# Optimization experiments

Hardware: AMD Instinct MI355X
Metric: run time of the kernel (lower is better)

The kernel has to match this reference:

```python
import jax, jax.numpy as jnp
import numpy as np

N_HEAD = 16
QMIN, QMAX = 0.0, 255.0  # 8-bit asymmetric


def fake_quantize(x, scale, zp):
    # LearnableFakeQuantize (asymmetric, 8-bit) with straight-through round.
    q = x / scale + zp
    q = q + jax.lax.stop_gradient(jnp.round(q) - q)  # STE round
    q = jnp.clip(q, QMIN, QMAX)
    return (q - zp) * scale


def setup_inputs() -> dict:
    key = jax.random.key(0)
    ks = jax.random.split(key, 4)
    B, T, C = 2, 2048, 1024
    return {
        "hidden_states": jax.random.normal(ks[0], (B, T, C), jnp.float32),
        "W_attn": jax.random.normal(ks[1], (C, 3 * C), jnp.float32) * (1.0 / np.sqrt(C)),
        "b_attn": jnp.zeros((3 * C,), jnp.float32),
        "W_proj": jax.random.normal(ks[2], (C, C), jnp.float32) * (1.0 / np.sqrt(C)),
        "b_proj": jnp.zeros((C,), jnp.float32),
        "kv_scale": jnp.full((1,), 0.05, jnp.float32),
        "kv_zp": jnp.full((1,), 128.0, jnp.float32),
    }


def reference(hidden_states, W_attn, b_attn, W_proj, b_proj, kv_scale, kv_zp):
    B, T, C = hidden_states.shape
    H = N_HEAD
    D = C // H
    qkv = hidden_states @ W_attn + b_attn            # [B,T,3C]
    q, k, v = jnp.split(qkv, 3, axis=2)
    # [B,T,C] -> [B,H,T,D]
    q = q.reshape(B, T, H, D).transpose(0, 2, 1, 3)
    k = k.reshape(B, T, H, D).transpose(0, 2, 1, 3)
    v = v.reshape(B, T, H, D).transpose(0, 2, 1, 3)
    k = fake_quantize(k, kv_scale, kv_zp)
    v = fake_quantize(v, kv_scale, kv_zp)
    scores = jnp.einsum("bhqd,bhkd->bhqk", q, k) / jnp.sqrt(jnp.asarray(D, q.dtype))
    causal = jnp.tril(jnp.ones((T, T), bool))        # bias[:T,:T]
    scores = jnp.where(causal, scores, jnp.asarray(-jnp.inf, scores.dtype))
    attn = jax.nn.softmax(scores, axis=-1)
    out = jnp.einsum("bhqk,bhkd->bhqd", attn, v)     # [B,H,T,D]
    out = out.transpose(0, 2, 1, 3).reshape(B, T, C)
    return out @ W_proj + b_proj
```

## Files before the change

kernel.cpp:

```cpp
#include <hip/hip_runtime.h>
#include <math.h>

#define TB 2048
#define CC 1024
#define NH 16
#define HD 64

typedef __bf16 bf16x8 __attribute__((ext_vector_type(8)));
typedef __bf16 bf16x4 __attribute__((ext_vector_type(4)));
typedef float  f32x4  __attribute__((ext_vector_type(4)));

__device__ inline float exp2fast(float x) { return __builtin_amdgcn_exp2f(x); }

__device__ __forceinline__ void gl_lds16(const __bf16* g, __bf16* l) {
    __builtin_amdgcn_global_load_lds(
        (const __attribute__((address_space(1))) void*)g,
        (__attribute__((address_space(3))) void*)l, 16, 0, 0);
}

__global__ __launch_bounds__(256)
void prep_kernel(const float* __restrict__ hidden, __bf16* __restrict__ hb,
                 const float* __restrict__ Wa, __bf16* __restrict__ wat,
                 const float* __restrict__ Wp, __bf16* __restrict__ wpt)
{
    __shared__ __bf16 L[64][68];
    const int tid = threadIdx.x;
    const int bid = blockIdx.x;
    if (bid < 4096) {
        int i = (bid * 256 + tid) * 4;
        f32x4 v = *(const f32x4*)&hidden[i];
        bf16x4 o;
        o.x = (__bf16)v.x; o.y = (__bf16)v.y; o.z = (__bf16)v.z; o.w = (__bf16)v.w;
        *(bf16x4*)&hb[i] = o;
        return;
    }
    const float* src; __bf16* dst; int N, n0, k0;
    if (bid < 4096 + 768) {
        int t = bid - 4096;
        src = Wa; dst = wat; N = 3072;
        n0 = (t % 48) * 64; k0 = (t / 48) * 64;
    } else {
        int t = bid - 4864;
        src = Wp; dst = wpt; N = 1024;
        n0 = (t % 16) * 64; k0 = (t / 16) * 64;
    }
    #pragma unroll
    for (int i = 0; i < 4; i++) {
        int id = tid + i * 256;
        int r = id >> 4, c = (id & 15) * 4;
        f32x4 v = *(const f32x4*)&src[(size_t)(k0 + r) * N + n0 + c];
        bf16x4 o;
        o.x = (__bf16)v.x; o.y = (__bf16)v.y; o.z = (__bf16)v.z; o.w = (__bf16)v.w;
        *(bf16x4*)&L[r][c] = o;
    }
    __syncthreads();
    #pragma unroll
    for (int i = 0; i < 4; i++) {
        int id = tid + i * 256;
        int nr = id >> 4, kc = (id & 15) * 4;
        bf16x4 o;
        o.x = L[kc + 0][nr]; o.y = L[kc + 1][nr];
        o.z = L[kc + 2][nr]; o.w = L[kc + 3][nr];
        *(bf16x4*)&dst[(size_t)(n0 + nr) * 1024 + k0 + kc] = o;
    }
}

template<int BN, int MODE>
__global__ __launch_bounds__(256)
void gemm_bt(const __bf16* __restrict__ A, const __bf16* __restrict__ Bt,
             const float* __restrict__ bias,
             __bf16* __restrict__ o0, __bf16* __restrict__ o1,
             __bf16* __restrict__ o2, float* __restrict__ of,
             int M, int N, int K,
             const float* __restrict__ scp, const float* __restrict__ zpp)
{
    constexpr int NT = BN / 32;
    __shared__ __bf16 Asm[128][64];
    __shared__ __bf16 Bsm[BN][64];

    const int tid  = threadIdx.x;
    const int m0   = blockIdx.y * 128;
    const int n0   = blockIdx.x * BN;
    const int w    = tid >> 6, lane = tid & 63;
    const int wm   = (w & 1) * 64, wn = (w >> 1) * (BN / 2);
    const int r16  = lane & 15, quad = lane >> 4;
    const int srow = lane >> 3;
    const int scol = ((lane & 7) ^ srow) * 8;
    const int rsw  = r16 & 7;

    f32x4 acc[NT][4];
    #pragma unroll
    for (int i = 0; i < NT; i++)
        #pragma unroll
        for (int j = 0; j < 4; j++) acc[i][j] = 0.f;

    for (int k0 = 0; k0 < K; k0 += 64) {
        #pragma unroll
        for (int p = 0; p < 4; p++)
            gl_lds16(&A[(size_t)(m0 + w * 32 + p * 8 + srow) * K + k0 + scol],
                     &Asm[w * 32 + p * 8][0]);
        #pragma unroll
        for (int p = 0; p < BN / 32; p++)
            gl_lds16(&Bt[(size_t)(n0 + w * (BN / 4) + p * 8 + srow) * K + k0 + scol],
                     &Bsm[w * (BN / 4) + p * 8][0]);
        __syncthreads();

        #pragma unroll
        for (int ks = 0; ks < 2; ks++) {
            const int col = ((ks * 4 + quad) ^ rsw) * 8;
            bf16x8 af[4], bfr[NT];
            #pragma unroll
            for (int mt = 0; mt < 4; mt++)
                af[mt] = *(const bf16x8*)&Asm[wm + mt * 16 + r16][col];
            #pragma unroll
            for (int nt = 0; nt < NT; nt++)
                bfr[nt] = *(const bf16x8*)&Bsm[wn + nt * 16 + r16][col];
            #pragma unroll
            for (int nt = 0; nt < NT; nt++)
                #pragma unroll
                for (int mt = 0; mt < 4; mt++)
                    acc[nt][mt] = __builtin_amdgcn_mfma_f32_16x16x32_bf16(
                        bfr[nt], af[mt], acc[nt][mt], 0, 0, 0);
        }
        __syncthreads();
    }

    const float sc = scp[0];
    const float zp = zpp[0];

    #pragma unroll
    for (int nt = 0; nt < NT; nt++) {
        #pragma unroll
        for (int mt = 0; mt < 4; mt++) {
            int gm = m0 + wm + mt * 16 + r16;
            int gn = n0 + wn + nt * 16 + quad * 4;
            f32x4 val = acc[nt][mt] + *(const f32x4*)&bias[gn];
            if (MODE == 1) {
                *(f32x4*)&of[(size_t)gm * N + gn] = val;
            } else {
                int part = gn >> 10;
                int idx  = gn & 1023;
                int h = idx >> 6, d = idx & 63;
                int b = gm >> 11, t = gm & 2047;
                bf16x4 st;
                if (part == 0) {
                    size_t off = (((size_t)(b * NH + h)) * TB + t) * HD + d;
                    #pragma unroll
                    for (int r = 0; r < 4; r++)
                        st[r] = (__bf16)(val[r] * 0.18033688f);
                    *(bf16x4*)&o0[off] = st;
                } else {
                    #pragma unroll
                    for (int r = 0; r < 4; r++) {
                        float qv = val[r] / sc + zp;
                        qv = rintf(qv);
                        qv = fminf(fmaxf(qv, 0.f), 255.f);
                        st[r] = (__bf16)((qv - zp) * sc);
                    }
                    if (part == 1) {
                        size_t off = (((size_t)(b * NH + h)) * TB + t) * HD + d;
                        *(bf16x4*)&o1[off] = st;
                    } else {
                        size_t offv = (((size_t)(b * NH + h)) * HD + d) * TB + t;
                        #pragma unroll
                        for (int r = 0; r < 4; r++)
                            o2[offv + (size_t)r * TB] = st[r];
                    }
                }
            }
        }
    }
}

__global__ __launch_bounds__(256)
void attn_mfma(const __bf16* __restrict__ Q, const __bf16* __restrict__ Kg,
               const __bf16* __restrict__ Vt, __bf16* __restrict__ O)
{
    __shared__ alignas(16) __bf16 Ksm[64][72];
    __shared__ alignas(16) __bf16 Vsm[64][72];

    const int tid = threadIdx.x;
    const int qt  = 31 - (blockIdx.x >> 5);
    const int bh  = blockIdx.x & 31;
    const int q0  = qt * 64;
    const int w   = tid >> 6, lane = tid & 63;
    const int l15 = lane & 15, quad = lane >> 4;
    const int b   = bh >> 4, h = bh & 15;

    const int srow = tid >> 3;
    const int sseg = (tid & 7) * 8;
    const int p0 = ((srow >> 2) & 1) * 32 + ((srow >> 3) & 3) * 4 + (srow & 3);
    const int p1 = p0 + 16;

    const __bf16* Kbh = Kg + (size_t)bh * TB * HD;
    const __bf16* Vbh = Vt + (size_t)bh * HD * TB;

    const __bf16* Qrow = Q + ((size_t)bh * TB + q0 + w * 16 + l15) * HD;
    bf16x8 qf0 = *(const bf16x8*)&Qrow[quad * 8];
    bf16x8 qf1 = *(const bf16x8*)&Qrow[32 + quad * 8];

    bf16x8 af_l;
    {
        __bf16 v = (l15 == 0) ? (__bf16)1.0f : (__bf16)0.0f;
        #pragma unroll
        for (int j = 0; j < 8; j++) af_l[j] = v;
    }

    f32x4 acc_o[4], acc_l;
    #pragma unroll
    for (int nt = 0; nt < 4; nt++) acc_o[nt] = 0.f;
    acc_l = 0.f;
    float mrun = -3.0e38f;

    bf16x8 kpre0 = *(const bf16x8*)&Kbh[(size_t)srow * HD + sseg];
    bf16x8 kpre1 = *(const bf16x8*)&Kbh[(size_t)(32 + srow) * HD + sseg];
    bf16x8 vpre0 = *(const bf16x8*)&Vbh[(size_t)srow * TB + sseg];
    bf16x8 vpre1 = *(const bf16x8*)&Vbh[(size_t)(32 + srow) * TB + sseg];

    for (int kt = 0; kt <= qt; kt++) {
        __syncthreads();
        *(bf16x8*)&Ksm[p0][sseg]        = kpre0;
        *(bf16x8*)&Ksm[p1][sseg]        = kpre1;
        *(bf16x8*)&Vsm[srow][sseg]      = vpre0;
        *(bf16x8*)&Vsm[32 + srow][sseg] = vpre1;
        __syncthreads();

        if (kt < qt) {
            const __bf16* Kn = Kbh + (size_t)(kt + 1) * 64 * HD;
            kpre0 = *(const bf16x8*)&Kn[(size_t)srow * HD + sseg];
            kpre1 = *(const bf16x8*)&Kn[(size_t)(32 + srow) * HD + sseg];
            const int cb = (kt + 1) * 64;
            vpre0 = *(const bf16x8*)&Vbh[(size_t)srow * TB + cb + sseg];
            vpre1 = *(const bf16x8*)&Vbh[(size_t)(32 + srow) * TB + cb + sseg];
        }

        const int kbase = kt * 64;
        const int qlo   = q0 + w * 16;
        const int qmax  = qlo + 15;

        f32x4 s[4];
        #pragma unroll
        for (int nt = 0; nt < 4; nt++) s[nt] = 0.f;
        #pragma unroll
        for (int nt = 0; nt < 4; nt++) {
            const int kmin = kbase + (nt & 1) * 32 + ((nt >> 1) << 2);
            if (kmin > qmax) continue;
            bf16x8 kf0 = *(const bf16x8*)&Ksm[nt * 16 + l15][quad * 8];
            bf16x8 kf1 = *(const bf16x8*)&Ksm[nt * 16 + l15][32 + quad * 8];
            s[nt] = __builtin_amdgcn_mfma_f32_16x16x32_bf16(kf0, qf0, s[nt], 0, 0, 0);
            s[nt] = __builtin_amdgcn_mfma_f32_16x16x32_bf16(kf1, qf1, s[nt], 0, 0, 0);
        }

        if (kbase + 63 > qlo) {
            const int qg = qlo + l15;
            #pragma unroll
            for (int nt = 0; nt < 4; nt++) {
                const int koff = kbase + (nt & 1) * 32 + ((nt >> 1) << 2) + quad * 8;
                #pragma unroll
                for (int r = 0; r < 4; r++)
                    if (koff + r > qg) s[nt][r] = -3.0e38f;
            }
        }

        float mx = s[0][0];
        #pragma unroll
        for (int nt = 0; nt < 4; nt++)
            #pragma unroll
            for (int r = 0; r < 4; r++) mx = fmaxf(mx, s[nt][r]);
        mx = fmaxf(mx, __shfl_xor(mx, 16));
        mx = fmaxf(mx, __shfl_xor(mx, 32));

        float mnew  = fmaxf(mrun, mx);
        float alpha = exp2fast(mrun - mnew);
        mrun = mnew;
        #pragma unroll
        for (int nt = 0; nt < 4; nt++)
            #pragma unroll
            for (int r = 0; r < 4; r++) acc_o[nt][r] *= alpha;
        acc_l[0] *= alpha;

        float p[4][4];
        #pragma unroll
        for (int nt = 0; nt < 4; nt++)
            #pragma unroll
            for (int r = 0; r < 4; r++) p[nt][r] = exp2fast(s[nt][r] - mnew);

        bf16x8 pf0, pf1;
        #pragma unroll
        for (int j = 0; j < 4; j++) {
            pf0[j]     = (__bf16)p[0][j];
            pf0[4 + j] = (__bf16)p[2][j];
            pf1[j]     = (__bf16)p[1][j];
            pf1[4 + j] = (__bf16)p[3][j];
        }

        acc_l = __builtin_amdgcn_mfma_f32_16x16x32_bf16(af_l, pf0, acc_l, 0, 0, 0);
        acc_l = __builtin_amdgcn_mfma_f32_16x16x32_bf16(af_l, pf1, acc_l, 0, 0, 0);

        #pragma unroll
        for (int nt = 0; nt < 4; nt++) {
            bf16x8 vf0 = *(const bf16x8*)&Vsm[nt * 16 + l15][quad * 8];
            bf16x8 vf1 = *(const bf16x8*)&Vsm[nt * 16 + l15][32 + quad * 8];
            acc_o[nt] = __builtin_amdgcn_mfma_f32_16x16x32_bf16(vf0, pf0, acc_o[nt], 0, 0, 0);
            acc_o[nt] = __builtin_amdgcn_mfma_f32_16x16x32_bf16(vf1, pf1, acc_o[nt], 0, 0, 0);
        }
    }

    float lall = __shfl(acc_l[0], l15);
    float inv  = 1.f / lall;
    size_t trow = (size_t)(b * TB) + q0 + w * 16 + l15;
    #pragma unroll
    for (int nt = 0; nt < 4; nt++) {
        bf16x4 st;
        #pragma unroll
        for (int r = 0; r < 4; r++) st[r] = (__bf16)(acc_o[nt][r] * inv);
        *(bf16x4*)&O[trow * CC + h * HD + nt * 16 + quad * 4] = st;
    }
}

extern "C" void kernel_launch(void* const* d_in, const int* in_sizes, int n_in,
                              void* d_out, int out_size, void* d_ws, size_t ws_size,
                              hipStream_t stream) {
    (void)in_sizes; (void)n_in; (void)out_size; (void)ws_size;
    const float* hidden   = (const float*)d_in[0];
    const float* W_attn   = (const float*)d_in[1];
    const float* b_attn   = (const float*)d_in[2];
    const float* W_proj   = (const float*)d_in[3];
    const float* b_proj   = (const float*)d_in[4];
    const float* kv_scale = (const float*)d_in[5];
    const float* kv_zp    = (const float*)d_in[6];
    float* out = (float*)d_out;

    __bf16* hb  = (__bf16*)d_ws;
    __bf16* wat = hb  + (size_t)4096 * 1024;
    __bf16* wpt = wat + (size_t)3072 * 1024;
    __bf16* qws = wpt + (size_t)1024 * 1024;
    __bf16* kws = qws + (size_t)2 * NH * TB * HD;
    __bf16* vws = kws + (size_t)2 * NH * TB * HD;
    __bf16* ows = vws + (size_t)2 * NH * TB * HD;

    prep_kernel<<<5120, 256, 0, stream>>>(hidden, hb, W_attn, wat, W_proj, wpt);

    gemm_bt<128, 0><<<dim3(24, 32), 256, 0, stream>>>(
        hb, wat, b_attn, qws, kws, vws, nullptr, 4096, 3072, 1024, kv_scale, kv_zp);

    attn_mfma<<<dim3(1024), 256, 0, stream>>>(qws, kws, vws, ows);

    gemm_bt<64, 1><<<dim3(16, 32), 256, 0, stream>>>(
        ows, wpt, b_proj, nullptr, nullptr, nullptr, out, 4096, 1024, 1024,
        kv_scale, kv_zp);
}
```

Before: 184.3 us.

## Halve attention query tile to 32 rows with 2-wave blocks and skip rescale

Attention blocks now cover 32 query rows with two waves instead of 64 rows with four, doubling the grid to 2048 blocks. Each thread stages four K/V rows per tile, and the loop bound is derived from the 32-row tile. Rescaling of the accumulators is skipped when no lane's running max increased. The intent is finer-grained causal work for better load balance and occupancy, at the cost of each K/V tile being loaded by twice as many blocks.

```diff
diff --git a/kernel.cpp b/kernel.cpp
--- a/kernel.cpp
+++ b/kernel.cpp
@@ -172,7 +172,7 @@
     }
 }
 
-__global__ __launch_bounds__(256)
+__global__ __launch_bounds__(128)
 void attn_mfma(const __bf16* __restrict__ Q, const __bf16* __restrict__ Kg,
                const __bf16* __restrict__ Vt, __bf16* __restrict__ O)
 {
@@ -180,17 +180,24 @@
     __shared__ alignas(16) __bf16 Vsm[64][72];
 
     const int tid = threadIdx.x;
-    const int qt  = 31 - (blockIdx.x >> 5);
+    const int qt  = 63 - (blockIdx.x >> 5);
     const int bh  = blockIdx.x & 31;
-    const int q0  = qt * 64;
+    const int q0  = qt * 32;
+    const int ktmax = (q0 + 31) >> 6;
     const int w   = tid >> 6, lane = tid & 63;
     const int l15 = lane & 15, quad = lane >> 4;
     const int b   = bh >> 4, h = bh & 15;
 
     const int srow = tid >> 3;
     const int sseg = (tid & 7) * 8;
-    const int p0 = ((srow >> 2) & 1) * 32 + ((srow >> 3) & 3) * 4 + (srow & 3);
-    const int p1 = p0 + 16;
+    int prow[4];
+    #pragma unroll
+    for (int i = 0; i < 4; i++) {
+        int k = srow + 16 * i;
+        int kb = k & 31;
+        prow[i] = ((kb >> 2) & 1) * 32 + ((kb >> 3) & 3) * 4 + (kb & 3)
+                + (k >> 5) * 16;
+    }
 
     const __bf16* Kbh = Kg + (size_t)bh * TB * HD;
     const __bf16* Vbh = Vt + (size_t)bh * HD * TB;
@@ -206,32 +213,36 @@
         for (int j = 0; j < 8; j++) af_l[j] = v;
     }
 
+    const f32x4 fzero = {0.f, 0.f, 0.f, 0.f};
     f32x4 acc_o[4], acc_l;
     #pragma unroll
-    for (int nt = 0; nt < 4; nt++) acc_o[nt] = 0.f;
-    acc_l = 0.f;
+    for (int nt = 0; nt < 4; nt++) acc_o[nt] = fzero;
+    acc_l = fzero;
     float mrun = -3.0e38f;
 
-    bf16x8 kpre0 = *(const bf16x8*)&Kbh[(size_t)srow * HD + sseg];
-    bf16x8 kpre1 = *(const bf16x8*)&Kbh[(size_t)(32 + srow) * HD + sseg];
-    bf16x8 vpre0 = *(const bf16x8*)&Vbh[(size_t)srow * TB + sseg];
-    bf16x8 vpre1 = *(const bf16x8*)&Vbh[(size_t)(32 + srow) * TB + sseg];
-
-    for (int kt = 0; kt <= qt; kt++) {
+    bf16x8 kpre[4], vpre[4];
+    #pragma unroll
+    for (int i = 0; i < 4; i++) {
+        kpre[i] = *(const bf16x8*)&Kbh[(size_t)(srow + 16 * i) * HD + sseg];
+        vpre[i] = *(const bf16x8*)&Vbh[(size_t)(srow + 16 * i) * TB + sseg];
+    }
+
+    for (int kt = 0; kt <= ktmax; kt++) {
         __syncthreads();
-        *(bf16x8*)&Ksm[p0][sseg]        = kpre0;
-        *(bf16x8*)&Ksm[p1][sseg]        = kpre1;
-        *(bf16x8*)&Vsm[srow][sseg]      = vpre0;
-        *(bf16x8*)&Vsm[32 + srow][sseg] = vpre1;
+        #pragma unroll
+        for (int i = 0; i < 4; i++) {
+            *(bf16x8*)&Ksm[prow[i]][sseg]       = kpre[i];
+            *(bf16x8*)&Vsm[srow + 16 * i][sseg] = vpre[i];
+        }
         __syncthreads();
 
-        if (kt < qt) {
-            const __bf16* Kn = Kbh + (size_t)(kt + 1) * 64 * HD;
-            kpre0 = *(const bf16x8*)&Kn[(size_t)srow * HD + sseg];
-            kpre1 = *(const bf16x8*)&Kn[(size_t)(32 + srow) * HD + sseg];
+        if (kt < ktmax) {
             const int cb = (kt + 1) * 64;
-            vpre0 = *(const bf16x8*)&Vbh[(size_t)srow * TB + cb + sseg];
-            vpre1 = *(const bf16x8*)&Vbh[(size_t)(32 + srow) * TB + cb + sseg];
+            #pragma unroll
+            for (int i = 0; i < 4; i++) {
+                kpre[i] = *(const bf16x8*)&Kbh[(size_t)(cb + srow + 16 * i) * HD + sseg];
+                vpre[i] = *(const bf16x8*)&Vbh[(size_t)(srow + 16 * i) * TB + cb + sseg];
+            }
         }
 
         const int kbase = kt * 64;
@@ -240,14 +251,12 @@
 
         f32x4 s[4];
         #pragma unroll
-        for (int nt = 0; nt < 4; nt++) s[nt] = 0.f;
-        #pragma unroll
         for (int nt = 0; nt < 4; nt++) {
             const int kmin = kbase + (nt & 1) * 32 + ((nt >> 1) << 2);
-            if (kmin > qmax) continue;
+            if (kmin > qmax) { s[nt] = fzero; continue; }
             bf16x8 kf0 = *(const bf16x8*)&Ksm[nt * 16 + l15][quad * 8];
             bf16x8 kf1 = *(const bf16x8*)&Ksm[nt * 16 + l15][32 + quad * 8];
-            s[nt] = __builtin_amdgcn_mfma_f32_16x16x32_bf16(kf0, qf0, s[nt], 0, 0, 0);
+            s[nt] = __builtin_amdgcn_mfma_f32_16x16x32_bf16(kf0, qf0, fzero, 0, 0, 0);
             s[nt] = __builtin_amdgcn_mfma_f32_16x16x32_bf16(kf1, qf1, s[nt], 0, 0, 0);
         }
 
@@ -270,14 +279,16 @@
         mx = fmaxf(mx, __shfl_xor(mx, 16));
         mx = fmaxf(mx, __shfl_xor(mx, 32));
 
-        float mnew  = fmaxf(mrun, mx);
-        float alpha = exp2fast(mrun - mnew);
+        float mnew = fmaxf(mrun, mx);
+        if (__any(mx > mrun)) {
+            float alpha = exp2fast(mrun - mnew);
+            #pragma unroll
+            for (int nt = 0; nt < 4; nt++)
+                #pragma unroll
+                for (int r = 0; r < 4; r++) acc_o[nt][r] *= alpha;
+            acc_l[0] *= alpha;
+        }
         mrun = mnew;
-        #pragma unroll
-        for (int nt = 0; nt < 4; nt++)
-            #pragma unroll
-            for (int r = 0; r < 4; r++) acc_o[nt][r] *= alpha;
-        acc_l[0] *= alpha;
 
         float p[4][4];
         #pragma unroll
@@ -344,7 +355,7 @@
     gemm_bt<128, 0><<<dim3(24, 32), 256, 0, stream>>>(
         hb, wat, b_attn, qws, kws, vws, nullptr, 4096, 3072, 1024, kv_scale, kv_zp);
 
-    attn_mfma<<<dim3(1024), 256, 0, stream>>>(qws, kws, vws, ows);
+    attn_mfma<<<dim3(2048), 128, 0, stream>>>(qws, kws, vws, ows);
 
     gemm_bt<64, 1><<<dim3(16, 32), 256, 0, stream>>>(
         ows, wpt, b_proj, nullptr, nullptr, nullptr, out, 4096, 1024, 1024,
```

Measured after the change: 187.8 us. Within noise of the previous version (+1.9%).
